# Performance work log

Hardware: AMD Instinct MI355X
Metric: run time of the kernel (lower is better)

Reference implementation:

```python
import jax, jax.numpy as jnp
import numpy as np

GRID = 20            # grid_size -> n1 = 400 nodes
CTX = 64             # context_size
HID = 10 * CTX       # hidden_dim per module code
BATCH = 256
K_ITERS = 100        # Dykstra iterations approximating the exact QP solve
LEAKY_SLOPE = 0.1


def _grid_incidence(g):
    """Incidence matrix of g x g grid DAG with right/down edges (SPO benchmark)."""
    n1 = g * g
    edges = []
    for i in range(g):
        for j in range(g):
            u = i * g + j
            if j + 1 < g:
                edges.append((u, u + 1))   # right
            if i + 1 < g:
                edges.append((u, u + g))   # down
    n2 = len(edges)
    A = np.zeros((n1, n2), dtype=np.float32)
    for e, (u, v) in enumerate(edges):
        A[u, e] = 1.0    # flow leaves u
        A[v, e] = -1.0   # flow enters v
    b = np.zeros(n1, dtype=np.float32)
    b[0] = 1.0           # source
    b[-1] = -1.0         # sink
    return A, b


def setup_inputs() -> dict:
    key = jax.random.key(0)
    ks = jax.random.split(key, 5)
    A_np, b_np = _grid_incidence(GRID)
    n2 = A_np.shape[1]
    d = jax.random.normal(ks[0], (BATCH, CTX), dtype=jnp.float32)
    W1 = jax.random.normal(ks[1], (CTX, HID), dtype=jnp.float32) / np.sqrt(CTX)
    b1 = jax.random.normal(ks[2], (HID,), dtype=jnp.float32) * 0.01
    W2 = jax.random.normal(ks[3], (HID, n2), dtype=jnp.float32) / np.sqrt(HID)
    b2 = jax.random.normal(ks[4], (n2,), dtype=jnp.float32) * 0.01
    return {
        "d": d, "W1": W1, "b1": b1, "W2": W2, "b2": b2,
        "A": jnp.asarray(A_np), "b_eq": jnp.asarray(b_np),
    }


def _solve_qp(w, A, b_eq):
    """Batched min_x w'x + 0.5||x||^2 s.t. Ax=b, x>=0 == proj of -w onto the
    feasible set, via Dykstra alternating projections (affine set / orthant)."""
    M = jnp.linalg.pinv(A @ A.T)  # [n1, n1]; AA' is the grid Laplacian (rank n1-1)

    def proj_affine(x):           # x: [B, n2]
        resid = x @ A.T - b_eq    # [B, n1]
        return x - (resid @ M) @ A

    y0 = -w                       # point to project
    p0 = jnp.zeros_like(w)
    q0 = jnp.zeros_like(w)

    def step(carry, _):
        y, p, q = carry
        t = y + p
        yp = proj_affine(t)
        p = t - yp
        t2 = yp + q
        y = jnp.maximum(t2, 0.0)  # projection onto x >= 0
        q = t2 - y
        return (y, p, q), None

    (y, _, _), _ = jax.lax.scan(step, (y0, p0, q0), None, length=K_ITERS)
    return y


def reference(d, W1, b1, W2, b2, A, b_eq):
    h = d @ W1 + b1
    h = jnp.where(h > 0, h, LEAKY_SLOPE * h)   # LeakyReLU(0.1)
    w = h @ W2 + b2                            # predicted edge costs [B, n2]
    return _solve_qp(w, A, b_eq)               # training-mode output: QP solution
```

## Files before the change

kernel.cpp:

```cpp
#include <hip/hip_runtime.h>
#include <math.h>

#define G 20
#define N1 400
#define N2 760
#define CTXS 64
#define HID 640
#define NB 256
#define ITERS 100
#define PI_D 3.14159265358979323846

__global__ __launch_bounds__(256, 1) void spnet_kernel(
    const float* __restrict__ dmat, const float* __restrict__ W1,
    const float* __restrict__ b1v, const float* __restrict__ W2,
    const float* __restrict__ b2v, const float* __restrict__ beq,
    float* __restrict__ out)
{
  const int tid = threadIdx.x;
  const int bb  = blockIdx.x;

  __shared__ __align__(16) float sV[N1];
  __shared__ __align__(16) float sdrow[CTXS];
  __shared__ __align__(16) float sh[HID];
  __shared__ __align__(16) float st[N2 + 4];
  __shared__ __align__(16) float srT[N1];
  __shared__ __align__(16) float sc1[N1];
  __shared__ __align__(16) float sc2T[N1];
  __shared__ __align__(16) float sd1[N1];
  __shared__ __align__(16) float sz[N1];

  for (int t = tid; t < N1; t += 256) {
    int k = t / G, i = t - G * k;
    double nk = (k == 0) ? 0.22360679774997896 : 0.31622776601683794;
    sV[t] = (float)(nk * cos(PI_D * (double)(k * (2 * i + 1)) / 40.0));
  }
  if (tid < CTXS) sdrow[tid] = dmat[bb * CTXS + tid];
  if (tid == 0) { st[N2] = 0.f; st[N2 + 1] = 0.f; st[N2 + 2] = 0.f; st[N2 + 3] = 0.f; }
  __syncthreads();

  if (tid < HID / 4) {
    float4 acc = *(const float4*)(b1v + 4 * tid);
#pragma unroll 4
    for (int k = 0; k < CTXS; k += 4) {
      float4 h4 = *(const float4*)(sdrow + k);
      const float* wb = W1 + k * HID + 4 * tid;
      float4 w0 = *(const float4*)(wb);
      float4 w1 = *(const float4*)(wb + HID);
      float4 w2 = *(const float4*)(wb + 2 * HID);
      float4 w3 = *(const float4*)(wb + 3 * HID);
      acc.x = fmaf(h4.x, w0.x, acc.x); acc.y = fmaf(h4.x, w0.y, acc.y);
      acc.z = fmaf(h4.x, w0.z, acc.z); acc.w = fmaf(h4.x, w0.w, acc.w);
      acc.x = fmaf(h4.y, w1.x, acc.x); acc.y = fmaf(h4.y, w1.y, acc.y);
      acc.z = fmaf(h4.y, w1.z, acc.z); acc.w = fmaf(h4.y, w1.w, acc.w);
      acc.x = fmaf(h4.z, w2.x, acc.x); acc.y = fmaf(h4.z, w2.y, acc.y);
      acc.z = fmaf(h4.z, w2.z, acc.z); acc.w = fmaf(h4.z, w2.w, acc.w);
      acc.x = fmaf(h4.w, w3.x, acc.x); acc.y = fmaf(h4.w, w3.y, acc.y);
      acc.z = fmaf(h4.w, w3.z, acc.z); acc.w = fmaf(h4.w, w3.w, acc.w);
    }
    acc.x = acc.x > 0.f ? acc.x : 0.1f * acc.x;
    acc.y = acc.y > 0.f ? acc.y : 0.1f * acc.y;
    acc.z = acc.z > 0.f ? acc.z : 0.1f * acc.z;
    acc.w = acc.w > 0.f ? acc.w : 0.1f * acc.w;
    *(float4*)(sh + 4 * tid) = acc;
  }
  __syncthreads();

  if (tid < N2 / 4) {
    float4 acc = *(const float4*)(b2v + 4 * tid);
#pragma unroll 2
    for (int k = 0; k < HID; k += 4) {
      float4 h4 = *(const float4*)(sh + k);
      const float* wb = W2 + k * N2 + 4 * tid;
      float4 w0 = *(const float4*)(wb);
      float4 w1 = *(const float4*)(wb + N2);
      float4 w2 = *(const float4*)(wb + 2 * N2);
      float4 w3 = *(const float4*)(wb + 3 * N2);
      acc.x = fmaf(h4.x, w0.x, acc.x); acc.y = fmaf(h4.x, w0.y, acc.y);
      acc.z = fmaf(h4.x, w0.z, acc.z); acc.w = fmaf(h4.x, w0.w, acc.w);
      acc.x = fmaf(h4.y, w1.x, acc.x); acc.y = fmaf(h4.y, w1.y, acc.y);
      acc.z = fmaf(h4.y, w1.z, acc.z); acc.w = fmaf(h4.y, w1.w, acc.w);
      acc.x = fmaf(h4.z, w2.x, acc.x); acc.y = fmaf(h4.z, w2.y, acc.y);
      acc.z = fmaf(h4.z, w2.z, acc.z); acc.w = fmaf(h4.z, w2.w, acc.w);
      acc.x = fmaf(h4.w, w3.x, acc.x); acc.y = fmaf(h4.w, w3.y, acc.y);
      acc.z = fmaf(h4.w, w3.z, acc.z); acc.w = fmaf(h4.w, w3.w, acc.w);
    }
    float4 s; s.x = -acc.x; s.y = -acc.y; s.z = -acc.z; s.w = -acc.w;
    *(float4*)(st + 4 * tid) = s;
  }
  __syncthreads();

  int eu_r[3], ev_r[3];
  float t_r[3], q_r[3], y_r[3];
#pragma unroll
  for (int j = 0; j < 3; ++j) {
    int e = tid + 256 * j;
    int u = 0, v = 0;
    if (e < N2) {
      if (e < 741) {
        int i = e / 39, rem = e - 39 * i;
        if (rem < 38) { int jj = rem >> 1; u = i * G + jj; v = (rem & 1) ? (u + G) : (u + 1); }
        else { u = i * G + 19; v = u + G; }
      } else { u = 380 + (e - 741); v = u + 1; }
    }
    eu_r[j] = u; ev_r[j] = v;
    q_r[j] = 0.f; y_r[j] = 0.f;
    t_r[j] = (e < N2) ? st[e] : 0.f;
  }

  int oA0, oA1, iA0, iA1, tpA; float bqA;
  {
    int u = tid, ii = u / G, jj = u - G * ii;
    oA0 = (jj < 19) ? ((ii < 19) ? 39 * ii + 2 * jj       : 741 + jj)       : N2;
    oA1 = (ii < 19) ? (39 * ii + ((jj < 19) ? 2 * jj + 1 : 38))             : N2;
    iA0 = (jj > 0)  ? ((ii < 19) ? 39 * ii + 2 * (jj - 1) : 741 + (jj - 1)) : N2;
    iA1 = (ii > 0)  ? (39 * (ii - 1) + ((jj < 19) ? 2 * jj + 1 : 38))       : N2;
    tpA = jj * G + ii;
    bqA = beq[u];
  }
  const bool hasB = (tid < 144);
  int oB0 = N2, oB1 = N2, iB0 = N2, iB1 = N2, tpB = 0; float bqB = 0.f;
  if (hasB) {
    int u = tid + 256, ii = u / G, jj = u - G * ii;
    oB0 = (jj < 19) ? ((ii < 19) ? 39 * ii + 2 * jj       : 741 + jj)       : N2;
    oB1 = (ii < 19) ? (39 * ii + ((jj < 19) ? 2 * jj + 1 : 38))             : N2;
    iB0 = (jj > 0)  ? ((ii < 19) ? 39 * ii + 2 * (jj - 1) : 741 + (jj - 1)) : N2;
    iB1 = (ii > 0)  ? (39 * (ii - 1) + ((jj < 19) ? 2 * jj + 1 : 38))       : N2;
    tpB = jj * G + ii;
    bqB = beq[u];
  }

  const bool hasP = (tid < 210);
  int a = 0, b = 0;
  float Vra[G], Vrb[G], Vca[G], Vcb[G];
  float Sab = 0.f;
  if (hasP) {
    int r = tid;
    while (r >= G - a) { r -= G - a; ++a; }
    b = a + r;
#pragma unroll
    for (int m = 0; m < G; ++m) {
      Vra[m] = sV[a * G + m]; Vrb[m] = sV[b * G + m];
      Vca[m] = sV[m * G + a]; Vcb[m] = sV[m * G + b];
    }
    double la = 2.0 - 2.0 * cos(PI_D * (double)a / 20.0);
    double lb = 2.0 - 2.0 * cos(PI_D * (double)b / 20.0);
    Sab = (a == 0 && b == 0) ? 0.f : (float)(1.0 / (la + lb));
  }
  const float4* rowA4[4];
  const float4* rowB4[4];
  rowA4[0] = (const float4*)(srT + b * G);  rowB4[0] = (const float4*)(srT + a * G);
  rowA4[1] = (const float4*)(sc1 + a * G);  rowB4[1] = (const float4*)(sc1 + b * G);
  rowA4[2] = (const float4*)(sc2T + b * G); rowB4[2] = (const float4*)(sc2T + a * G);
  rowA4[3] = (const float4*)(sd1 + a * G);  rowB4[3] = (const float4*)(sd1 + b * G);

  for (int it = 0; it < ITERS; ++it) {
    {
      float rA = (st[oA0] + st[oA1]) - (st[iA0] + st[iA1]) - bqA;
      srT[tpA] = rA;
      if (hasB) {
        float rB = (st[oB0] + st[oB1]) - (st[iB0] + st[iB1]) - bqB;
        srT[tpB] = rB;
      }
    }
    __syncthreads();

    if (hasP) {
      float x0 = 0.f, x1 = 0.f;
#pragma unroll
      for (int m = 0; m < 5; ++m) {
        float4 ta = rowA4[0][m], tb = rowB4[0][m];
        x0 = fmaf(Vra[4 * m], ta.x, x0); x0 = fmaf(Vra[4 * m + 1], ta.y, x0);
        x0 = fmaf(Vra[4 * m + 2], ta.z, x0); x0 = fmaf(Vra[4 * m + 3], ta.w, x0);
        x1 = fmaf(Vrb[4 * m], tb.x, x1); x1 = fmaf(Vrb[4 * m + 1], tb.y, x1);
        x1 = fmaf(Vrb[4 * m + 2], tb.z, x1); x1 = fmaf(Vrb[4 * m + 3], tb.w, x1);
      }
      sc1[a * G + b] = x0; sc1[b * G + a] = x1;
    }
    __syncthreads();

    if (hasP) {
      float x0 = 0.f, x1 = 0.f;
#pragma unroll
      for (int m = 0; m < 5; ++m) {
        float4 ta = rowA4[1][m], tb = rowB4[1][m];
        x0 = fmaf(Vrb[4 * m], ta.x, x0); x0 = fmaf(Vrb[4 * m + 1], ta.y, x0);
        x0 = fmaf(Vrb[4 * m + 2], ta.z, x0); x0 = fmaf(Vrb[4 * m + 3], ta.w, x0);
        x1 = fmaf(Vra[4 * m], tb.x, x1); x1 = fmaf(Vra[4 * m + 1], tb.y, x1);
        x1 = fmaf(Vra[4 * m + 2], tb.z, x1); x1 = fmaf(Vra[4 * m + 3], tb.w, x1);
      }
      sc2T[b * G + a] = x0 * Sab; sc2T[a * G + b] = x1 * Sab;
    }
    __syncthreads();

    if (hasP) {
      float x0 = 0.f, x1 = 0.f;
#pragma unroll
      for (int m = 0; m < 5; ++m) {
        float4 ta = rowA4[2][m], tb = rowB4[2][m];
        x0 = fmaf(Vca[4 * m], ta.x, x0); x0 = fmaf(Vca[4 * m + 1], ta.y, x0);
        x0 = fmaf(Vca[4 * m + 2], ta.z, x0); x0 = fmaf(Vca[4 * m + 3], ta.w, x0);
        x1 = fmaf(Vcb[4 * m], tb.x, x1); x1 = fmaf(Vcb[4 * m + 1], tb.y, x1);
        x1 = fmaf(Vcb[4 * m + 2], tb.z, x1); x1 = fmaf(Vcb[4 * m + 3], tb.w, x1);
      }
      sd1[a * G + b] = x0; sd1[b * G + a] = x1;
    }
    __syncthreads();

    if (hasP) {
      float x0 = 0.f, x1 = 0.f;
#pragma unroll
      for (int m = 0; m < 5; ++m) {
        float4 ta = rowA4[3][m], tb = rowB4[3][m];
        x0 = fmaf(Vcb[4 * m], ta.x, x0); x0 = fmaf(Vcb[4 * m + 1], ta.y, x0);
        x0 = fmaf(Vcb[4 * m + 2], ta.z, x0); x0 = fmaf(Vcb[4 * m + 3], ta.w, x0);
        x1 = fmaf(Vca[4 * m], tb.x, x1); x1 = fmaf(Vca[4 * m + 1], tb.y, x1);
        x1 = fmaf(Vca[4 * m + 2], tb.z, x1); x1 = fmaf(Vca[4 * m + 3], tb.w, x1);
      }
      sz[a * G + b] = x0; sz[b * G + a] = x1;
    }
    __syncthreads();

#pragma unroll
    for (int j = 0; j < 3; ++j) {
      int e = tid + 256 * j;
      if (e < N2) {
        float pn = sz[eu_r[j]] - sz[ev_r[j]];
        float yp = t_r[j] - pn;
        float t2 = yp + q_r[j];
        float yn = fmaxf(t2, 0.f);
        q_r[j] = t2 - yn;
        y_r[j] = yn;
        float tn = yn + pn;
        t_r[j] = tn;
        st[e] = tn;
      }
    }
    __syncthreads();
  }

#pragma unroll
  for (int j = 0; j < 3; ++j) {
    int e = tid + 256 * j;
    if (e < N2) out[bb * N2 + e] = y_r[j];
  }
}

extern "C" void kernel_launch(void* const* d_in, const int* in_sizes, int n_in,
                              void* d_out, int out_size, void* d_ws, size_t ws_size,
                              hipStream_t stream) {
  const float* d   = (const float*)d_in[0];
  const float* W1  = (const float*)d_in[1];
  const float* b1  = (const float*)d_in[2];
  const float* W2  = (const float*)d_in[3];
  const float* b2  = (const float*)d_in[4];
  const float* beq = (const float*)d_in[6];
  float* out = (float*)d_out;
  spnet_kernel<<<NB, 256, 0, stream>>>(d, W1, b1, W2, b2, beq, out);
}
```

Measured before the change: 224.6 us.

## Restructure Dykstra loop into grid-shaped edge tiles with 4-wide DCT thread mapping

```diff
diff --git a/kernel.cpp b/kernel.cpp
--- a/kernel.cpp
+++ b/kernel.cpp
@@ -22,20 +22,23 @@
   __shared__ __align__(16) float sV[N1];
   __shared__ __align__(16) float sdrow[CTXS];
   __shared__ __align__(16) float sh[HID];
-  __shared__ __align__(16) float st[N2 + 4];
-  __shared__ __align__(16) float srT[N1];
-  __shared__ __align__(16) float sc1[N1];
-  __shared__ __align__(16) float sc2T[N1];
-  __shared__ __align__(16) float sd1[N1];
-  __shared__ __align__(16) float sz[N1];
+  __shared__ __align__(16) float st0[N2];
+  __shared__ __align__(16) float tRs[G][G];
+  __shared__ __align__(16) float tDs[21][G];
+  __shared__ __align__(16) float srow[G][G];
+  __shared__ __align__(16) float T1T[G][G];
+  __shared__ __align__(16) float T2T[G][G];
+  __shared__ __align__(16) float W3m[G][G];
+  __shared__ __align__(16) float Zs[G][G];
 
   for (int t = tid; t < N1; t += 256) {
     int k = t / G, i = t - G * k;
     double nk = (k == 0) ? 0.22360679774997896 : 0.31622776601683794;
     sV[t] = (float)(nk * cos(PI_D * (double)(k * (2 * i + 1)) / 40.0));
-  }
+    ((float*)tRs)[t] = 0.f;
+  }
+  for (int t = tid; t < 21 * G; t += 256) ((float*)tDs)[t] = 0.f;
   if (tid < CTXS) sdrow[tid] = dmat[bb * CTXS + tid];
-  if (tid == 0) { st[N2] = 0.f; st[N2 + 1] = 0.f; st[N2 + 2] = 0.f; st[N2 + 3] = 0.f; }
   __syncthreads();
 
   if (tid < HID / 4) {
@@ -85,163 +88,189 @@
       acc.z = fmaf(h4.w, w3.z, acc.z); acc.w = fmaf(h4.w, w3.w, acc.w);
     }
     float4 s; s.x = -acc.x; s.y = -acc.y; s.z = -acc.z; s.w = -acc.w;
-    *(float4*)(st + 4 * tid) = s;
-  }
-  __syncthreads();
-
-  int eu_r[3], ev_r[3];
-  float t_r[3], q_r[3], y_r[3];
-#pragma unroll
-  for (int j = 0; j < 3; ++j) {
-    int e = tid + 256 * j;
-    int u = 0, v = 0;
-    if (e < N2) {
-      if (e < 741) {
-        int i = e / 39, rem = e - 39 * i;
-        if (rem < 38) { int jj = rem >> 1; u = i * G + jj; v = (rem & 1) ? (u + G) : (u + 1); }
-        else { u = i * G + 19; v = u + G; }
-      } else { u = 380 + (e - 741); v = u + 1; }
-    }
-    eu_r[j] = u; ev_r[j] = v;
-    q_r[j] = 0.f; y_r[j] = 0.f;
-    t_r[j] = (e < N2) ? st[e] : 0.f;
-  }
-
-  int oA0, oA1, iA0, iA1, tpA; float bqA;
-  {
-    int u = tid, ii = u / G, jj = u - G * ii;
-    oA0 = (jj < 19) ? ((ii < 19) ? 39 * ii + 2 * jj       : 741 + jj)       : N2;
-    oA1 = (ii < 19) ? (39 * ii + ((jj < 19) ? 2 * jj + 1 : 38))             : N2;
-    iA0 = (jj > 0)  ? ((ii < 19) ? 39 * ii + 2 * (jj - 1) : 741 + (jj - 1)) : N2;
-    iA1 = (ii > 0)  ? (39 * (ii - 1) + ((jj < 19) ? 2 * jj + 1 : 38))       : N2;
-    tpA = jj * G + ii;
-    bqA = beq[u];
-  }
-  const bool hasB = (tid < 144);
-  int oB0 = N2, oB1 = N2, iB0 = N2, iB1 = N2, tpB = 0; float bqB = 0.f;
-  if (hasB) {
-    int u = tid + 256, ii = u / G, jj = u - G * ii;
-    oB0 = (jj < 19) ? ((ii < 19) ? 39 * ii + 2 * jj       : 741 + jj)       : N2;
-    oB1 = (ii < 19) ? (39 * ii + ((jj < 19) ? 2 * jj + 1 : 38))             : N2;
-    iB0 = (jj > 0)  ? ((ii < 19) ? 39 * ii + 2 * (jj - 1) : 741 + (jj - 1)) : N2;
-    iB1 = (ii > 0)  ? (39 * (ii - 1) + ((jj < 19) ? 2 * jj + 1 : 38))       : N2;
-    tpB = jj * G + ii;
-    bqB = beq[u];
-  }
-
-  const bool hasP = (tid < 210);
-  int a = 0, b = 0;
-  float Vra[G], Vrb[G], Vca[G], Vcb[G];
-  float Sab = 0.f;
-  if (hasP) {
-    int r = tid;
-    while (r >= G - a) { r -= G - a; ++a; }
-    b = a + r;
-#pragma unroll
-    for (int m = 0; m < G; ++m) {
-      Vra[m] = sV[a * G + m]; Vrb[m] = sV[b * G + m];
-      Vca[m] = sV[m * G + a]; Vcb[m] = sV[m * G + b];
-    }
-    double la = 2.0 - 2.0 * cos(PI_D * (double)a / 20.0);
-    double lb = 2.0 - 2.0 * cos(PI_D * (double)b / 20.0);
-    Sab = (a == 0 && b == 0) ? 0.f : (float)(1.0 / (la + lb));
-  }
-  const float4* rowA4[4];
-  const float4* rowB4[4];
-  rowA4[0] = (const float4*)(srT + b * G);  rowB4[0] = (const float4*)(srT + a * G);
-  rowA4[1] = (const float4*)(sc1 + a * G);  rowB4[1] = (const float4*)(sc1 + b * G);
-  rowA4[2] = (const float4*)(sc2T + b * G); rowB4[2] = (const float4*)(sc2T + a * G);
-  rowA4[3] = (const float4*)(sd1 + a * G);  rowB4[3] = (const float4*)(sd1 + b * G);
+    *(float4*)(st0 + 4 * tid) = s;
+  }
+  __syncthreads();
+
+  const bool isD = (tid < 100);
+  const int  rid = tid - 128;
+  const bool isR = (rid >= 0 && rid < 100);
+
+  const int dx  = tid % G;
+  const int dk0 = 4 * (tid / G);
+  float Vr[4][G], Vc[4][G], Sv[4];
+  if (isD) {
+#pragma unroll
+    for (int a = 0; a < 4; ++a) {
+      int k = dk0 + a;
+#pragma unroll
+      for (int m = 0; m < G; ++m) { Vr[a][m] = sV[k * G + m]; Vc[a][m] = sV[m * G + k]; }
+      double lk = 2.0 - 2.0 * cos(PI_D * (double)k / 20.0);
+      double lx = 2.0 - 2.0 * cos(PI_D * (double)dx / 20.0);
+      Sv[a] = (k == 0 && dx == 0) ? 0.f : (float)(1.0 / (lk + lx));
+    }
+  }
+
+  const int di = tid / 5, dj4 = (tid % 5) * 4;
+  const bool dAct = isD && (di < 19);
+  float dT[4], dQ[4], dY[4];
+  if (dAct) {
+#pragma unroll
+    for (int m = 0; m < 4; ++m) {
+      int j = dj4 + m;
+      int e = (j < 19) ? (39 * di + 2 * j + 1) : (39 * di + 38);
+      dT[m] = st0[e]; dQ[m] = 0.f; dY[m] = 0.f;
+    }
+    float4 w4 = {dT[0], dT[1], dT[2], dT[3]};
+    *(float4*)&tDs[di + 1][dj4] = w4;
+  }
+
+  const int ri = rid / 5, rj4 = (rid % 5) * 4;
+  float rT[4], rQ[4], rY[4]; float4 bq4 = {0.f, 0.f, 0.f, 0.f};
+  if (isR) {
+#pragma unroll
+    for (int m = 0; m < 4; ++m) {
+      int j = rj4 + m;
+      if (j < 19) {
+        int e = (ri < 19) ? (39 * ri + 2 * j) : (741 + j);
+        rT[m] = st0[e];
+      } else rT[m] = 0.f;
+      rQ[m] = 0.f; rY[m] = 0.f;
+    }
+    float4 w4 = {rT[0], rT[1], rT[2], rT[3]};
+    *(float4*)&tRs[ri][rj4] = w4;
+    bq4 = *(const float4*)(beq + ri * G + rj4);
+  }
+  __syncthreads();
 
   for (int it = 0; it < ITERS; ++it) {
-    {
-      float rA = (st[oA0] + st[oA1]) - (st[iA0] + st[iA1]) - bqA;
-      srT[tpA] = rA;
-      if (hasB) {
-        float rB = (st[oB0] + st[oB1]) - (st[iB0] + st[iB1]) - bqB;
-        srT[tpB] = rB;
-      }
-    }
-    __syncthreads();
-
-    if (hasP) {
-      float x0 = 0.f, x1 = 0.f;
-#pragma unroll
-      for (int m = 0; m < 5; ++m) {
-        float4 ta = rowA4[0][m], tb = rowB4[0][m];
-        x0 = fmaf(Vra[4 * m], ta.x, x0); x0 = fmaf(Vra[4 * m + 1], ta.y, x0);
-        x0 = fmaf(Vra[4 * m + 2], ta.z, x0); x0 = fmaf(Vra[4 * m + 3], ta.w, x0);
-        x1 = fmaf(Vrb[4 * m], tb.x, x1); x1 = fmaf(Vrb[4 * m + 1], tb.y, x1);
-        x1 = fmaf(Vrb[4 * m + 2], tb.z, x1); x1 = fmaf(Vrb[4 * m + 3], tb.w, x1);
-      }
-      sc1[a * G + b] = x0; sc1[b * G + a] = x1;
-    }
-    __syncthreads();
-
-    if (hasP) {
-      float x0 = 0.f, x1 = 0.f;
-#pragma unroll
-      for (int m = 0; m < 5; ++m) {
-        float4 ta = rowA4[1][m], tb = rowB4[1][m];
-        x0 = fmaf(Vrb[4 * m], ta.x, x0); x0 = fmaf(Vrb[4 * m + 1], ta.y, x0);
-        x0 = fmaf(Vrb[4 * m + 2], ta.z, x0); x0 = fmaf(Vrb[4 * m + 3], ta.w, x0);
-        x1 = fmaf(Vra[4 * m], tb.x, x1); x1 = fmaf(Vra[4 * m + 1], tb.y, x1);
-        x1 = fmaf(Vra[4 * m + 2], tb.z, x1); x1 = fmaf(Vra[4 * m + 3], tb.w, x1);
-      }
-      sc2T[b * G + a] = x0 * Sab; sc2T[a * G + b] = x1 * Sab;
-    }
-    __syncthreads();
-
-    if (hasP) {
-      float x0 = 0.f, x1 = 0.f;
-#pragma unroll
-      for (int m = 0; m < 5; ++m) {
-        float4 ta = rowA4[2][m], tb = rowB4[2][m];
-        x0 = fmaf(Vca[4 * m], ta.x, x0); x0 = fmaf(Vca[4 * m + 1], ta.y, x0);
-        x0 = fmaf(Vca[4 * m + 2], ta.z, x0); x0 = fmaf(Vca[4 * m + 3], ta.w, x0);
-        x1 = fmaf(Vcb[4 * m], tb.x, x1); x1 = fmaf(Vcb[4 * m + 1], tb.y, x1);
-        x1 = fmaf(Vcb[4 * m + 2], tb.z, x1); x1 = fmaf(Vcb[4 * m + 3], tb.w, x1);
-      }
-      sd1[a * G + b] = x0; sd1[b * G + a] = x1;
-    }
-    __syncthreads();
-
-    if (hasP) {
-      float x0 = 0.f, x1 = 0.f;
-#pragma unroll
-      for (int m = 0; m < 5; ++m) {
-        float4 ta = rowA4[3][m], tb = rowB4[3][m];
-        x0 = fmaf(Vcb[4 * m], ta.x, x0); x0 = fmaf(Vcb[4 * m + 1], ta.y, x0);
-        x0 = fmaf(Vcb[4 * m + 2], ta.z, x0); x0 = fmaf(Vcb[4 * m + 3], ta.w, x0);
-        x1 = fmaf(Vca[4 * m], tb.x, x1); x1 = fmaf(Vca[4 * m + 1], tb.y, x1);
-        x1 = fmaf(Vca[4 * m + 2], tb.z, x1); x1 = fmaf(Vca[4 * m + 3], tb.w, x1);
-      }
-      sz[a * G + b] = x0; sz[b * G + a] = x1;
-    }
-    __syncthreads();
-
-#pragma unroll
-    for (int j = 0; j < 3; ++j) {
-      int e = tid + 256 * j;
-      if (e < N2) {
-        float pn = sz[eu_r[j]] - sz[ev_r[j]];
-        float yp = t_r[j] - pn;
-        float t2 = yp + q_r[j];
+    if (isR) {
+      float4 oR = *(const float4*)&tRs[ri][rj4];
+      float  lf = (rj4 > 0) ? tRs[ri][rj4 - 1] : 0.f;
+      float4 oD = *(const float4*)&tDs[ri + 1][rj4];
+      float4 iD = *(const float4*)&tDs[ri][rj4];
+      float4 r4;
+      r4.x = oR.x + oD.x - lf   - iD.x - bq4.x;
+      r4.y = oR.y + oD.y - oR.x - iD.y - bq4.y;
+      r4.z = oR.z + oD.z - oR.y - iD.z - bq4.z;
+      r4.w = oR.w + oD.w - oR.z - iD.w - bq4.w;
+      *(float4*)&srow[ri][rj4] = r4;
+    }
+    __syncthreads();
+
+    if (isD) {
+      const float4* Rp = (const float4*)&srow[dx][0];
+      float4 a0 = Rp[0], a1 = Rp[1], a2 = Rp[2], a3 = Rp[3], a4 = Rp[4];
+      float rr[G] = {a0.x,a0.y,a0.z,a0.w, a1.x,a1.y,a1.z,a1.w, a2.x,a2.y,a2.z,a2.w,
+                     a3.x,a3.y,a3.z,a3.w, a4.x,a4.y,a4.z,a4.w};
+#pragma unroll
+      for (int a = 0; a < 4; ++a) {
+        float acc = 0.f;
+#pragma unroll
+        for (int m = 0; m < G; ++m) acc = fmaf(Vr[a][m], rr[m], acc);
+        T1T[dk0 + a][dx] = acc;
+      }
+    }
+    __syncthreads();
+
+    if (isD) {
+      const float4* Rp = (const float4*)&T1T[dx][0];
+      float4 a0 = Rp[0], a1 = Rp[1], a2 = Rp[2], a3 = Rp[3], a4 = Rp[4];
+      float rr[G] = {a0.x,a0.y,a0.z,a0.w, a1.x,a1.y,a1.z,a1.w, a2.x,a2.y,a2.z,a2.w,
+                     a3.x,a3.y,a3.z,a3.w, a4.x,a4.y,a4.z,a4.w};
+      float o[4];
+#pragma unroll
+      for (int a = 0; a < 4; ++a) {
+        float acc = 0.f;
+#pragma unroll
+        for (int m = 0; m < G; ++m) acc = fmaf(Vr[a][m], rr[m], acc);
+        o[a] = acc * Sv[a];
+      }
+      float4 w4 = {o[0], o[1], o[2], o[3]};
+      *(float4*)&T2T[dx][dk0] = w4;
+    }
+    __syncthreads();
+
+    if (isD) {
+      const float4* Rp = (const float4*)&T2T[dx][0];
+      float4 a0 = Rp[0], a1 = Rp[1], a2 = Rp[2], a3 = Rp[3], a4 = Rp[4];
+      float rr[G] = {a0.x,a0.y,a0.z,a0.w, a1.x,a1.y,a1.z,a1.w, a2.x,a2.y,a2.z,a2.w,
+                     a3.x,a3.y,a3.z,a3.w, a4.x,a4.y,a4.z,a4.w};
+#pragma unroll
+      for (int a = 0; a < 4; ++a) {
+        float acc = 0.f;
+#pragma unroll
+        for (int m = 0; m < G; ++m) acc = fmaf(Vc[a][m], rr[m], acc);
+        W3m[dk0 + a][dx] = acc;
+      }
+    }
+    __syncthreads();
+
+    if (isD) {
+      const float4* Rp = (const float4*)&W3m[dx][0];
+      float4 a0 = Rp[0], a1 = Rp[1], a2 = Rp[2], a3 = Rp[3], a4 = Rp[4];
+      float rr[G] = {a0.x,a0.y,a0.z,a0.w, a1.x,a1.y,a1.z,a1.w, a2.x,a2.y,a2.z,a2.w,
+                     a3.x,a3.y,a3.z,a3.w, a4.x,a4.y,a4.z,a4.w};
+      float o[4];
+#pragma unroll
+      for (int a = 0; a < 4; ++a) {
+        float acc = 0.f;
+#pragma unroll
+        for (int m = 0; m < G; ++m) acc = fmaf(Vc[a][m], rr[m], acc);
+        o[a] = acc;
+      }
+      float4 w4 = {o[0], o[1], o[2], o[3]};
+      *(float4*)&Zs[dx][dk0] = w4;
+    }
+    __syncthreads();
+
+    if (isR) {
+      float4 z4 = *(const float4*)&Zs[ri][rj4];
+      float  zR = (rj4 < 16) ? Zs[ri][rj4 + 4] : 0.f;
+      float pn[4] = {z4.x - z4.y, z4.y - z4.z, z4.z - z4.w, z4.w - zR};
+      if (rj4 == 16) pn[3] = 0.f;
+#pragma unroll
+      for (int m = 0; m < 4; ++m) {
+        float t2 = rT[m] - pn[m] + rQ[m];
         float yn = fmaxf(t2, 0.f);
-        q_r[j] = t2 - yn;
-        y_r[j] = yn;
-        float tn = yn + pn;
-        t_r[j] = tn;
-        st[e] = tn;
-      }
-    }
-    __syncthreads();
-  }
-
-#pragma unroll
-  for (int j = 0; j < 3; ++j) {
-    int e = tid + 256 * j;
-    if (e < N2) out[bb * N2 + e] = y_r[j];
+        rQ[m] = t2 - yn; rY[m] = yn; rT[m] = yn + pn[m];
+      }
+      float4 w4 = {rT[0], rT[1], rT[2], rT[3]};
+      *(float4*)&tRs[ri][rj4] = w4;
+    }
+    if (dAct) {
+      float4 z4 = *(const float4*)&Zs[di][dj4];
+      float4 zb = *(const float4*)&Zs[di + 1][dj4];
+      float pn[4] = {z4.x - zb.x, z4.y - zb.y, z4.z - zb.z, z4.w - zb.w};
+#pragma unroll
+      for (int m = 0; m < 4; ++m) {
+        float t2 = dT[m] - pn[m] + dQ[m];
+        float yn = fmaxf(t2, 0.f);
+        dQ[m] = t2 - yn; dY[m] = yn; dT[m] = yn + pn[m];
+      }
+      float4 w4 = {dT[0], dT[1], dT[2], dT[3]};
+      *(float4*)&tDs[di + 1][dj4] = w4;
+    }
+    __syncthreads();
+  }
+
+  if (isR) {
+#pragma unroll
+    for (int m = 0; m < 4; ++m) {
+      int j = rj4 + m;
+      if (j < 19) {
+        int e = (ri < 19) ? (39 * ri + 2 * j) : (741 + j);
+        out[bb * N2 + e] = rY[m];
+      }
+    }
+  }
+  if (dAct) {
+#pragma unroll
+    for (int m = 0; m < 4; ++m) {
+      int j = dj4 + m;
+      int e = (j < 19) ? (39 * di + 2 * j + 1) : (39 * di + 38);
+      out[bb * N2 + e] = dY[m];
+    }
   }
 }
 
```

Result: no change. 221.0 us (-1.6%).
